# Kernel tuning notes

Measured on AMD Instinct MI355X. Metric: run time of the kernel, lower is better.

The kernel has to match this reference:

```python
import jax, jax.numpy as jnp
import numpy as np

N = 100000
E = 3200000
F_IN = 128
H1 = 16
H2 = 8
NEG_SLOPE = 0.2


def _gat_layer(x, src, dst, W, a_src, a_dst, b, n_nodes):
    # x: [N, Fin]; src/dst: [E_tot] (self-loops included); W: [Fin, Fout]
    h = x @ W                                   # [N, Fout]
    e_src = h @ a_src                           # [N]
    e_dst = h @ a_dst                           # [N]
    e = e_src[src] + e_dst[dst]                 # [E_tot]
    e = jnp.where(e > 0, e, NEG_SLOPE * e)      # leaky_relu(0.2)
    m = jax.ops.segment_max(e, dst, num_segments=n_nodes)   # [N]
    w = jnp.exp(e - m[dst])                     # [E_tot]
    s = jax.ops.segment_sum(w, dst, num_segments=n_nodes)   # [N]
    alpha = w / s[dst]                          # [E_tot]
    out = jax.ops.segment_sum(alpha[:, None] * h[src], dst, num_segments=n_nodes)
    return out + b


def setup_inputs() -> dict:
    key = jax.random.key(0)
    ks = jax.random.split(key, 12)
    x = jax.random.normal(ks[0], (N, F_IN), dtype=jnp.float32)
    edge_index = jax.random.randint(ks[1], (E, 2), 0, N, dtype=jnp.int64)
    s1 = 1.0 / np.sqrt(F_IN)
    s2 = 1.0 / np.sqrt(H1)
    s3 = 1.0 / np.sqrt(H2)
    return {
        "x": x,
        "edge_index": edge_index,
        "W1": jax.random.normal(ks[2], (F_IN, H1), dtype=jnp.float32) * s1,
        "a1_src": jax.random.normal(ks[3], (H1,), dtype=jnp.float32) * s2,
        "a1_dst": jax.random.normal(ks[4], (H1,), dtype=jnp.float32) * s2,
        "b1": jnp.zeros((H1,), dtype=jnp.float32),
        "W2": jax.random.normal(ks[5], (H1, H2), dtype=jnp.float32) * s2,
        "a2_src": jax.random.normal(ks[6], (H2,), dtype=jnp.float32) * s3,
        "a2_dst": jax.random.normal(ks[7], (H2,), dtype=jnp.float32) * s3,
        "b2": jnp.zeros((H2,), dtype=jnp.float32),
        "Wf": jax.random.normal(ks[8], (H2, 1), dtype=jnp.float32) * s3,
        "bf": jnp.zeros((1,), dtype=jnp.float32),
    }


def reference(x, edge_index, W1, a1_src, a1_dst, b1, W2, a2_src, a2_dst, b2, Wf, bf):
    ei = edge_index.T                            # [2, E] as in original forward
    loop = jnp.arange(N, dtype=ei.dtype)
    src = jnp.concatenate([ei[0], loop])         # PyG add_self_loops=True
    dst = jnp.concatenate([ei[1], loop])
    h = jax.nn.relu(_gat_layer(x, src, dst, W1, a1_src, a1_dst, b1, N))
    # dropout p=0.05 is identity at inference
    h = jax.nn.relu(_gat_layer(h, src, dst, W2, a2_src, a2_dst, b2, N))
    return h @ Wf + bf                           # [N, 1]
```

## Files before the change

### kernel.cpp

```cpp
#include <hip/hip_runtime.h>
#include <math.h>

#define N_NODES 100000
#define N_EDGES 3200000
#define E_TOT   (N_EDGES + N_NODES)
#define F_IN    128
#define H1      16
#define H2      8
#define NEG     0.2f
#define NBUCKET ((N_NODES + 255) >> 8)
#define NCHUNK  512
#define CE      ((N_EDGES + NCHUNK - 1) / NCHUNK)

typedef _Float16 half4v __attribute__((ext_vector_type(4)));
typedef _Float16 half8v __attribute__((ext_vector_type(8)));

__global__ __launch_bounds__(256) void k1_xw(
        const float* __restrict__ x, const float* __restrict__ W1,
        const float* __restrict__ a1s, const float* __restrict__ a1d,
        char* __restrict__ g1, float* __restrict__ e1d) {
    __shared__ float w1s[F_IN * H1];
    __shared__ float xs[16 * 132];
    __shared__ float a1ss[H1], a1ds[H1];
    const int tid = threadIdx.x;
    for (int i = tid; i < F_IN * H1; i += 256) w1s[i] = W1[i];
    if (tid < H1) { a1ss[tid] = a1s[tid]; a1ds[tid] = a1d[tid]; }
    const int rowbase = blockIdx.x * 16;
    #pragma unroll
    for (int i = 0; i < 2; i++) {
        int q = tid + i * 256;
        int r = q >> 5, c = q & 31;
        float4 v = *(const float4*)(x + (size_t)(rowbase + r) * F_IN + c * 4);
        *(float4*)(xs + r * 132 + c * 4) = v;
    }
    __syncthreads();
    const int g = tid >> 4, j = tid & 15;
    const float* xrow = xs + g * 132;
    float acc = 0.f;
    #pragma unroll 8
    for (int k = 0; k < F_IN; k++) acc += xrow[k] * w1s[k * H1 + j];
    const int row = rowbase + g;
    char* grow = g1 + (size_t)row * 64;
    ((_Float16*)grow)[j] = (_Float16)acc;
    float ps = acc * a1ss[j];
    float pd = acc * a1ds[j];
    #pragma unroll
    for (int m = 8; m >= 1; m >>= 1) {
        ps += __shfl_xor(ps, m, 16);
        pd += __shfl_xor(pd, m, 16);
    }
    if (j == 0) { *(float*)(grow + 32) = ps; e1d[row] = pd; }
}


__global__ __launch_bounds__(256) void k_count(const int2* __restrict__ ei,
                                               int* __restrict__ counts) {
    __shared__ int hist[NBUCKET];
    for (int i = threadIdx.x; i < NBUCKET; i += 256) hist[i] = 0;
    __syncthreads();
    const int b = blockIdx.x;
    const int beg = b * CE, end = min(N_EDGES, beg + CE);
    for (int e = beg + threadIdx.x; e < end; e += 256)
        atomicAdd(&hist[ei[e].y >> 8], 1);
    __syncthreads();
    for (int i = threadIdx.x; i < NBUCKET; i += 256)
        counts[i * NCHUNK + b] = hist[i];
}

__global__ __launch_bounds__(512) void k_scanA(int* __restrict__ counts,
                                               int* __restrict__ btot) {
    __shared__ int lds[NCHUNK];
    const int k = blockIdx.x, t = threadIdx.x;
    int v = counts[k * NCHUNK + t];
    lds[t] = v;
    __syncthreads();
    for (int off = 1; off < NCHUNK; off <<= 1) {
        int u = (t >= off) ? lds[t - off] : 0;
        __syncthreads();
        lds[t] += u;
        __syncthreads();
    }
    counts[k * NCHUNK + t] = lds[t] - v;
    if (t == NCHUNK - 1) btot[k] = lds[t];
}

__global__ __launch_bounds__(512) void k_scanB(const int* __restrict__ btot,
                                               int* __restrict__ bbase) {
    __shared__ int lds[512];
    const int t = threadIdx.x;
    int v = (t < NBUCKET) ? btot[t] : 0;
    lds[t] = v;
    __syncthreads();
    for (int off = 1; off < 512; off <<= 1) {
        int u = (t >= off) ? lds[t - off] : 0;
        __syncthreads();
        lds[t] += u;
        __syncthreads();
    }
    if (t < NBUCKET) bbase[t] = lds[t] - v;
    if (t == 511) bbase[NBUCKET] = lds[511];
}

__global__ __launch_bounds__(256) void k_reorder(const int2* __restrict__ ei,
                                                 const int* __restrict__ counts,
                                                 const int* __restrict__ bbase,
                                                 int* __restrict__ pairs) {
    __shared__ int cur[NBUCKET];
    const int b = blockIdx.x;
    for (int i = threadIdx.x; i < NBUCKET; i += 256)
        cur[i] = bbase[i] + counts[i * NCHUNK + b];
    __syncthreads();
    const int beg = b * CE, end = min(N_EDGES, beg + CE);
    for (int e = beg + threadIdx.x; e < end; e += 256) {
        int2 v = ei[e];
        int k = v.y >> 8;
        int pos = atomicAdd(&cur[k], 1);
        pairs[pos] = (v.x << 8) | (v.y & 255);
    }
}

__global__ __launch_bounds__(256) void k_csr(const int* __restrict__ pairs,
                                             const int* __restrict__ bbase,
                                             int* __restrict__ rowg,
                                             int* __restrict__ degg,
                                             int* __restrict__ sorted_src) {
    __shared__ int deg[256], scn[256], cur[256];
    const int k = blockIdx.x, t = threadIdx.x;
    const int n0 = k << 8;
    const int nn = min(256, N_NODES - n0);
    deg[t] = 0;
    __syncthreads();
    const int ebeg = bbase[k], eend = bbase[k + 1];
    for (int e = ebeg + t; e < eend; e += 256)
        atomicAdd(&deg[pairs[e] & 255], 1);
    __syncthreads();
    int v = (t < nn) ? deg[t] : 0;
    scn[t] = v;
    __syncthreads();
    for (int off = 1; off < 256; off <<= 1) {
        int u = (t >= off) ? scn[t - off] : 0;
        __syncthreads();
        scn[t] += u;
        __syncthreads();
    }
    int excl = scn[t] - v;
    if (t < nn) {
        int r = ebeg + excl + n0 + t;
        rowg[n0 + t] = r;
        degg[n0 + t] = v + 1;
        sorted_src[r] = n0 + t;
        cur[t] = r + 1;
    }
    __syncthreads();
    for (int e = ebeg + t; e < eend; e += 256) {
        int p = pairs[e];
        int pos = atomicAdd(&cur[p & 255], 1);
        sorted_src[pos] = p >> 8;
    }
}

template <int LPN, int U, int ROWB, int ESOFF, bool LAYER2>
__global__ __launch_bounds__(256) void k_agg(
        const int* __restrict__ row, const int* __restrict__ deg,
        const int* __restrict__ sorted_src,
        const float* __restrict__ ed, const char* __restrict__ gtab,
        const float* __restrict__ b,
        const float* __restrict__ W2, const float* __restrict__ a2s,
        const float* __restrict__ a2d,
        char* __restrict__ g2out, float* __restrict__ e2d_out,
        const float* __restrict__ Wf, const float* __restrict__ bf,
        float* __restrict__ out) {
    __shared__ float w2s[H1 * H2];
    __shared__ float a2ss[H2], a2ds[H2];
    if (!LAYER2) {
        for (int i = threadIdx.x; i < H1 * H2; i += 256) w2s[i] = W2[i];
        if (threadIdx.x < H2) { a2ss[threadIdx.x] = a2s[threadIdx.x];
                                a2ds[threadIdx.x] = a2d[threadIdx.x]; }
        __syncthreads();
    }
    const int sub = threadIdx.x & (LPN - 1);
    const int node = (blockIdx.x * 256 + threadIdx.x) / LPN;
    if (node >= N_NODES) return;
    const int beg = row[node];
    const int cnt = deg[node];
    const float edv = ed[node];
    float4 acc = make_float4(0.f, 0.f, 0.f, 0.f);
    float s = 0.f;
    for (int t0 = 0; t0 < cnt; t0 += U) {
        int srcs[U];
        float evs[U];
        half4v hvs[U];
        #pragma unroll
        for (int i = 0; i < U; i++) {
            int idx = t0 + i;
            srcs[i] = sorted_src[beg + (idx < cnt ? idx : 0)];
        }
        #pragma unroll
        for (int i = 0; i < U; i++) {
            const char* rp = gtab + (size_t)srcs[i] * ROWB;
            hvs[i] = *(const half4v*)(rp + sub * 8);
            evs[i] = *(const float*)(rp + ESOFF);
        }
        #pragma unroll
        for (int i = 0; i < U; i++) {
            if (t0 + i < cnt) {
                float e = evs[i] + edv;
                e = e > 0.f ? e : NEG * e;
                float p = __expf(e);
                s += p;
                acc.x += p * (float)hvs[i].x;
                acc.y += p * (float)hvs[i].y;
                acc.z += p * (float)hvs[i].z;
                acc.w += p * (float)hvs[i].w;
            }
        }
    }
    const float inv = 1.f / s;
    const float4 b4 = ((const float4*)b)[sub];
    float4 o;
    o.x = fmaxf(acc.x * inv + b4.x, 0.f);
    o.y = fmaxf(acc.y * inv + b4.y, 0.f);
    o.z = fmaxf(acc.z * inv + b4.z, 0.f);
    o.w = fmaxf(acc.w * inv + b4.w, 0.f);
    if (!LAYER2) {
        float p2[H2];
        const float* wrow = w2s + (sub * 4) * H2;
        #pragma unroll
        for (int i = 0; i < H2; i++)
            p2[i] = o.x * wrow[i] + o.y * wrow[H2 + i]
                  + o.z * wrow[2 * H2 + i] + o.w * wrow[3 * H2 + i];
        #pragma unroll
        for (int i = 0; i < H2; i++) {
            p2[i] += __shfl_xor(p2[i], 1);
            p2[i] += __shfl_xor(p2[i], 2);
        }
        float es2 = 0.f, ed2 = 0.f;
        #pragma unroll
        for (int i = 0; i < H2; i++) { es2 += p2[i] * a2ss[i]; ed2 += p2[i] * a2ds[i]; }
        char* orow = g2out + (size_t)node * 32;
        if (sub == 0) {
            half8v h8;
            #pragma unroll
            for (int i = 0; i < H2; i++) h8[i] = (_Float16)p2[i];
            *(half8v*)orow = h8;
        } else if (sub == 1) {
            *(float*)(orow + 16) = es2;
        } else if (sub == 2) {
            e2d_out[node] = ed2;
        }
    } else {
        const float4 w4 = ((const float4*)Wf)[sub];
        float r = o.x * w4.x + o.y * w4.y + o.z * w4.z + o.w * w4.w;
        r += __shfl_xor(r, 1);
        if (sub == 0) out[node] = r + bf[0];
    }
}

extern "C" void kernel_launch(void* const* d_in, const int* in_sizes, int n_in,
                              void* d_out, int out_size, void* d_ws, size_t ws_size,
                              hipStream_t stream) {
    const float* x    = (const float*)d_in[0];
    const int2*  ei   = (const int2*)d_in[1];
    const float* W1   = (const float*)d_in[2];
    const float* a1s  = (const float*)d_in[3];
    const float* a1d  = (const float*)d_in[4];
    const float* b1   = (const float*)d_in[5];
    const float* W2   = (const float*)d_in[6];
    const float* a2s  = (const float*)d_in[7];
    const float* a2d  = (const float*)d_in[8];
    const float* b2   = (const float*)d_in[9];
    const float* Wf   = (const float*)d_in[10];
    const float* bf   = (const float*)d_in[11];
    float* out = (float*)d_out;

    char* wp = (char*)d_ws;
    int* sorted_src = (int*)wp;   wp += sizeof(int) * (size_t)E_TOT;
    char* pairs_region = wp;      wp += sizeof(int) * (size_t)N_EDGES;
    int* counts     = (int*)wp;   wp += sizeof(int) * (size_t)NBUCKET * NCHUNK;
    int* btot       = (int*)wp;   wp += sizeof(int) * (NBUCKET + 1);
    int* bbase      = (int*)wp;   wp += sizeof(int) * (NBUCKET + 1);
    int* degg       = (int*)wp;   wp += sizeof(int) * N_NODES;
    int* rowg       = (int*)wp;   wp += sizeof(int) * N_NODES;

    int*   pairs = (int*)pairs_region;
    char*  g1    = pairs_region;
    char*  g2    = pairs_region + (size_t)64 * N_NODES;
    float* e1d   = (float*)(g2 + (size_t)32 * N_NODES);
    float* e2d   = e1d + N_NODES;

    k_count<<<NCHUNK, 256, 0, stream>>>(ei, counts);
    k_scanA<<<NBUCKET, 512, 0, stream>>>(counts, btot);
    k_scanB<<<1, 512, 0, stream>>>(btot, bbase);
    k_reorder<<<NCHUNK, 256, 0, stream>>>(ei, counts, bbase, pairs);
    k_csr<<<NBUCKET, 256, 0, stream>>>(pairs, bbase, rowg, degg, sorted_src);
    k1_xw<<<N_NODES / 16, 256, 0, stream>>>(x, W1, a1s, a1d, g1, e1d);
    k_agg<4, 8, 64, 32, false><<<(N_NODES * 4 + 255) / 256, 256, 0, stream>>>(
        rowg, degg, sorted_src, e1d, g1, b1, W2, a2s, a2d, g2, e2d,
        nullptr, nullptr, nullptr);
    k_agg<2, 8, 32, 16, true><<<(N_NODES * 2 + 255) / 256, 256, 0, stream>>>(
        rowg, degg, sorted_src, e2d, g2, b2, nullptr, nullptr, nullptr,
        nullptr, nullptr, Wf, bf, out);
}
```

Measured before the change: 288.6 us.

## Double lanes per node in aggregation and prefetch next source indices

Aggregation kernels now use twice as many lanes per node, each handling two half-precision features instead of four, with an extra shuffle stage added to the reductions. The source-index loads for the next group of U edges are issued before the current group's math, overlapping index fetch latency with the gather. Row offsets now use 32-bit unsigned multiplication. This raises parallelism per node but duplicates the exp and edge-score work across more lanes and doubles thread count.

```diff
diff --git a/kernel.cpp b/kernel.cpp
--- a/kernel.cpp
+++ b/kernel.cpp
@@ -12,7 +12,7 @@
 #define NCHUNK  512
 #define CE      ((N_EDGES + NCHUNK - 1) / NCHUNK)
 
-typedef _Float16 half4v __attribute__((ext_vector_type(4)));
+typedef _Float16 half2v __attribute__((ext_vector_type(2)));
 typedef _Float16 half8v __attribute__((ext_vector_type(8)));
 
 __global__ __launch_bounds__(256) void k1_xw(
@@ -184,22 +184,25 @@
     const int beg = row[node];
     const int cnt = deg[node];
     const float edv = ed[node];
-    float4 acc = make_float4(0.f, 0.f, 0.f, 0.f);
+    float2 acc = make_float2(0.f, 0.f);
     float s = 0.f;
+    int srcs[U];
+    #pragma unroll
+    for (int i = 0; i < U; i++) srcs[i] = sorted_src[beg + (i < cnt ? i : 0)];
     for (int t0 = 0; t0 < cnt; t0 += U) {
-        int srcs[U];
         float evs[U];
-        half4v hvs[U];
+        half2v hvs[U];
         #pragma unroll
         for (int i = 0; i < U; i++) {
-            int idx = t0 + i;
-            srcs[i] = sorted_src[beg + (idx < cnt ? idx : 0)];
-        }
+            const char* rp = gtab + (unsigned)srcs[i] * ROWB;
+            hvs[i] = *(const half2v*)(rp + sub * 4);
+            evs[i] = *(const float*)(rp + ESOFF);
+        }
+        int nsrcs[U];
         #pragma unroll
         for (int i = 0; i < U; i++) {
-            const char* rp = gtab + (size_t)srcs[i] * ROWB;
-            hvs[i] = *(const half4v*)(rp + sub * 8);
-            evs[i] = *(const float*)(rp + ESOFF);
+            int idx = t0 + U + i;
+            nsrcs[i] = sorted_src[beg + (idx < cnt ? idx : 0)];
         }
         #pragma unroll
         for (int i = 0; i < U; i++) {
@@ -210,29 +213,27 @@
                 s += p;
                 acc.x += p * (float)hvs[i].x;
                 acc.y += p * (float)hvs[i].y;
-                acc.z += p * (float)hvs[i].z;
-                acc.w += p * (float)hvs[i].w;
             }
         }
+        #pragma unroll
+        for (int i = 0; i < U; i++) srcs[i] = nsrcs[i];
     }
     const float inv = 1.f / s;
-    const float4 b4 = ((const float4*)b)[sub];
-    float4 o;
-    o.x = fmaxf(acc.x * inv + b4.x, 0.f);
-    o.y = fmaxf(acc.y * inv + b4.y, 0.f);
-    o.z = fmaxf(acc.z * inv + b4.z, 0.f);
-    o.w = fmaxf(acc.w * inv + b4.w, 0.f);
+    const float2 bv = ((const float2*)b)[sub];
+    float2 o;
+    o.x = fmaxf(acc.x * inv + bv.x, 0.f);
+    o.y = fmaxf(acc.y * inv + bv.y, 0.f);
     if (!LAYER2) {
         float p2[H2];
-        const float* wrow = w2s + (sub * 4) * H2;
-        #pragma unroll
-        for (int i = 0; i < H2; i++)
-            p2[i] = o.x * wrow[i] + o.y * wrow[H2 + i]
-                  + o.z * wrow[2 * H2 + i] + o.w * wrow[3 * H2 + i];
+        const float* w0 = w2s + (2 * sub) * H2;
+        const float* w1 = w2s + (2 * sub + 1) * H2;
+        #pragma unroll
+        for (int i = 0; i < H2; i++) p2[i] = o.x * w0[i] + o.y * w1[i];
         #pragma unroll
         for (int i = 0; i < H2; i++) {
             p2[i] += __shfl_xor(p2[i], 1);
             p2[i] += __shfl_xor(p2[i], 2);
+            p2[i] += __shfl_xor(p2[i], 4);
         }
         float es2 = 0.f, ed2 = 0.f;
         #pragma unroll
@@ -249,9 +250,10 @@
             e2d_out[node] = ed2;
         }
     } else {
-        const float4 w4 = ((const float4*)Wf)[sub];
-        float r = o.x * w4.x + o.y * w4.y + o.z * w4.z + o.w * w4.w;
+        const float2 wv = ((const float2*)Wf)[sub];
+        float r = o.x * wv.x + o.y * wv.y;
         r += __shfl_xor(r, 1);
+        r += __shfl_xor(r, 2);
         if (sub == 0) out[node] = r + bf[0];
     }
 }
@@ -294,10 +296,10 @@
     k_reorder<<<NCHUNK, 256, 0, stream>>>(ei, counts, bbase, pairs);
     k_csr<<<NBUCKET, 256, 0, stream>>>(pairs, bbase, rowg, degg, sorted_src);
     k1_xw<<<N_NODES / 16, 256, 0, stream>>>(x, W1, a1s, a1d, g1, e1d);
-    k_agg<4, 8, 64, 32, false><<<(N_NODES * 4 + 255) / 256, 256, 0, stream>>>(
+    k_agg<8, 8, 64, 32, false><<<(N_NODES * 8 + 255) / 256, 256, 0, stream>>>(
         rowg, degg, sorted_src, e1d, g1, b1, W2, a2s, a2d, g2, e2d,
         nullptr, nullptr, nullptr);
-    k_agg<2, 8, 32, 16, true><<<(N_NODES * 2 + 255) / 256, 256, 0, stream>>>(
+    k_agg<4, 8, 32, 16, true><<<(N_NODES * 4 + 255) / 256, 256, 0, stream>>>(
         rowg, degg, sorted_src, e2d, g2, b2, nullptr, nullptr, nullptr,
         nullptr, nullptr, Wf, bf, out);
 }
```

Result: faster. 269.3 us (-6.7%).
